# Performance work log

Hardware: AMD Instinct MI355X
Metric: run time of the kernel (lower is better)

## Reference

```python
import jax, jax.numpy as jnp
import numpy as np

S = 7                # feature map size
A = 12               # anchors per cell
N = S * S * A        # 588 total anchors
ANCHOR_SCALES = [0.3, 0.5, 0.7, 0.9]
ANCHOR_RATIOS = [0.7, 1.0, 1.3]
CONF_THR = 0.3
NMS_THR = 0.5
MAX_DET = 100
BN_EPS = 1e-5
DN = ('NCHW', 'OIHW', 'NCHW')


def _anchors():
    g = (jnp.arange(S, dtype=jnp.float32) + 0.5) / S
    cx, cy = jnp.meshgrid(g, g, indexing='ij')
    centers = jnp.stack([cx, cy], -1).reshape(-1, 2)                 # [49,2]
    sc = jnp.asarray(ANCHOR_SCALES, jnp.float32)[:, None]
    rt = jnp.sqrt(jnp.asarray(ANCHOR_RATIOS, jnp.float32))[None, :]
    ws = (sc * rt).reshape(-1)
    hs = (sc / rt).reshape(-1)
    deltas = jnp.stack([-ws, -hs, ws, hs], -1) * 0.5                 # [12,4]
    return (jnp.concatenate([centers, centers], -1)[:, None, :] + deltas[None]).reshape(-1, 4)


def _conv(x, w, b, pad):
    y = jax.lax.conv_general_dilated(x, w, (1, 1), [(pad, pad), (pad, pad)], dimension_numbers=DN)
    return y + b[None, :, None, None]


def _bn_relu(x, g, be, mu, var):
    inv = g * jax.lax.rsqrt(var + BN_EPS)
    return jax.nn.relu(x * inv[None, :, None, None] + (be - mu * inv)[None, :, None, None])


def _decode(box_pred, anchors):
    ac = (anchors[:, :2] + anchors[:, 2:]) * 0.5
    asz = anchors[:, 2:] - anchors[:, :2]
    pc = box_pred[..., :2] * asz + ac
    ps = jnp.exp(box_pred[..., 2:]) * asz
    return jnp.concatenate([pc - ps * 0.5, pc + ps * 0.5], -1)


def _iou(b):
    area = (b[:, 2] - b[:, 0]) * (b[:, 3] - b[:, 1])
    lt = jnp.maximum(b[:, None, :2], b[None, :, :2])
    rb = jnp.minimum(b[:, None, 2:], b[None, :, 2:])
    wh = jnp.clip(rb - lt, 0.0)
    inter = wh[..., 0] * wh[..., 1]
    return inter / (area[:, None] + area[None, :] - inter + 1e-9)


def _nms_single(boxes, scores):
    # greedy NMS, fixed-shape: sort by score, sequentially suppress, pad to MAX_DET
    order = jnp.argsort(-scores)
    bs = boxes[order]
    ss = scores[order]
    vs = ss > CONF_THR
    iou = _iou(bs)
    idx = jnp.arange(N)

    def body(suppr, i):
        keep = vs[i] & jnp.logical_not(suppr[i])
        suppr = suppr | (keep & (iou[i] > NMS_THR) & (idx > i))
        return suppr, keep

    _, keep = jax.lax.scan(body, jnp.zeros((N,), bool), idx)
    kept = jnp.where(keep, ss, -1.0)           # scores in (0,1), -1 is a safe sentinel
    top_s, top_i = jax.lax.top_k(kept, MAX_DET)
    valid = top_s > 0.0
    out_b = jnp.where(valid[:, None], bs[top_i], 0.0)
    out_s = jnp.where(valid, top_s, 0.0)
    return jnp.concatenate([out_b, out_s[:, None], valid.astype(jnp.float32)[:, None]], -1)


def _forward(features, w1, b1, g1, be1, mu1, var1, w2, b2, g2, be2, mu2, var2,
             w3, b3, g3, be3, mu3, var3, w4, b4, g4, be4, mu4, var4,
             w_cls, b_cls, w_box, b_box):
    x = _bn_relu(_conv(features, w1, b1, 0), g1, be1, mu1, var1)   # fpn 1x1
    x = _bn_relu(_conv(x, w2, b2, 1), g2, be2, mu2, var2)          # fpn 3x3
    x = _bn_relu(_conv(x, w3, b3, 1), g3, be3, mu3, var3)          # det_conv 1
    x = _bn_relu(_conv(x, w4, b4, 1), g4, be4, mu4, var4)          # det_conv 2
    B = features.shape[0]
    box = _conv(x, w_box, b_box, 1).transpose(0, 2, 3, 1).reshape(B, -1, 4)
    conf = jax.nn.sigmoid(_conv(x, w_cls, b_cls, 1)).transpose(0, 2, 3, 1).reshape(B, -1)
    boxes = _decode(box, _anchors())
    return jax.vmap(_nms_single)(boxes, conf)   # [B, MAX_DET, 6] = box(4)+score+valid


def setup_inputs() -> dict:
    key = jax.random.key(0)
    ks = iter(jax.random.split(key, 64))
    B = 256
    d = {'features': jax.random.normal(next(ks), (B, 512, S, S), jnp.float32)}
    for n, o, i, k in [('1', 256, 512, 1), ('2', 256, 256, 3), ('3', 256, 256, 3), ('4', 256, 256, 3)]:
        d['w' + n] = 0.01 * jax.random.normal(next(ks), (o, i, k, k), jnp.float32)
        d['b' + n] = jnp.zeros((o,), jnp.float32)
        d['g' + n] = 1.0 + 0.1 * jax.random.normal(next(ks), (o,), jnp.float32)
        d['be' + n] = 0.05 * jax.random.normal(next(ks), (o,), jnp.float32)
        d['mu' + n] = 0.1 * jax.random.normal(next(ks), (o,), jnp.float32)
        d['var' + n] = jax.random.uniform(next(ks), (o,), jnp.float32, 0.5, 1.5)
    d['w_cls'] = 0.01 * jax.random.normal(next(ks), (A, 256, 3, 3), jnp.float32)
    d['b_cls'] = jnp.zeros((A,), jnp.float32)
    d['w_box'] = 0.01 * jax.random.normal(next(ks), (4 * A, 256, 3, 3), jnp.float32)
    d['b_box'] = jnp.zeros((4 * A,), jnp.float32)
    return d


def reference(features, w1, b1, g1, be1, mu1, var1, w2, b2, g2, be2, mu2, var2,
              w3, b3, g3, be3, mu3, var3, w4, b4, g4, be4, mu4, var4,
              w_cls, b_cls, w_box, b_box):
    return _forward(features, w1, b1, g1, be1, mu1, var1, w2, b2, g2, be2, mu2, var2,
                    w3, b3, g3, be3, mu3, var3, w4, b4, g4, be4, mu4, var4,
                    w_cls, b_cls, w_box, b_box)
```

## Files before the change

### kernel.cpp

```cpp
#include <hip/hip_runtime.h>
#include <cmath>
#include <cstdint>

#define NPOS 49
#define NANCH 588

__global__ void transpose_all(
    const float* __restrict__ w1, const float* __restrict__ w2,
    const float* __restrict__ w3, const float* __restrict__ w4,
    const float* __restrict__ wb, const float* __restrict__ wc,
    float* __restrict__ w1t, float* __restrict__ w2t, float* __restrict__ w3t,
    float* __restrict__ w4t, float* __restrict__ wbt, float* __restrict__ wct) {
  int idx = blockIdx.x * blockDim.x + threadIdx.x;
  if (idx < 131072) {
    int o = idx / 512, c = idx % 512;
    w1t[((c >> 2) * 256 + o) * 4 + (c & 3)] = w1[idx];
    return;
  }
  idx -= 131072;
  if (idx < 589824) {
    int o = idx / 2304, ck = idx % 2304, c = ck / 9, k = ck - c * 9;
    w2t[(c * 256 + o) * 12 + k] = w2[idx]; return;
  }
  idx -= 589824;
  if (idx < 589824) {
    int o = idx / 2304, ck = idx % 2304, c = ck / 9, k = ck - c * 9;
    w3t[(c * 256 + o) * 12 + k] = w3[idx]; return;
  }
  idx -= 589824;
  if (idx < 589824) {
    int o = idx / 2304, ck = idx % 2304, c = ck / 9, k = ck - c * 9;
    w4t[(c * 256 + o) * 12 + k] = w4[idx]; return;
  }
  idx -= 589824;
  if (idx < 110592) { int o = idx / 2304, ck = idx % 2304; wbt[ck * 48 + o] = wb[idx]; return; }
  idx -= 110592;
  if (idx < 27648)  { int o = idx / 2304, ck = idx % 2304; wct[ck * 12 + o] = wc[idx]; return; }
}

__global__ __launch_bounds__(512, 1) void conv1x1_bn(
    const float* __restrict__ in, const float* __restrict__ wt_f,
    const float* __restrict__ bias, const float* __restrict__ gg,
    const float* __restrict__ be, const float* __restrict__ mu,
    const float* __restrict__ var, float* __restrict__ out) {
  __shared__ float smem[512 * 52];
  const int b = blockIdx.x, t = threadIdx.x;
  const int slot = t & 127, cg = t >> 7;
  const int o0 = slot, o1 = slot + 128;
  const float* inb = in + (size_t)b * (512 * NPOS);
  const float4* wq = (const float4*)wt_f;
  const int q0 = cg * 32;
  float4 wca = wq[q0 * 256 + o0];
  float4 wcb = wq[q0 * 256 + o1];
  for (int i = t; i < 512 * NPOS; i += 512) {
    int c = i / NPOS, p = i - c * NPOS;
    smem[c * 52 + p] = inb[i];
  }
  float acc0[NPOS], acc1[NPOS];
#pragma unroll
  for (int p = 0; p < NPOS; ++p) { acc0[p] = 0.f; acc1[p] = 0.f; }
  __syncthreads();
  for (int q = q0; q < q0 + 32; ++q) {
    int nq = (q + 1 < q0 + 32) ? q + 1 : q;
    float4 wna = wq[nq * 256 + o0];
    float4 wnb = wq[nq * 256 + o1];
#pragma unroll
    for (int j = 0; j < 4; ++j) {
      float wa = (j == 0) ? wca.x : (j == 1) ? wca.y : (j == 2) ? wca.z : wca.w;
      float wb2 = (j == 0) ? wcb.x : (j == 1) ? wcb.y : (j == 2) ? wcb.z : wcb.w;
      const float* row = smem + (q * 4 + j) * 52;
      const float4* tr = (const float4*)row;
#pragma unroll
      for (int jj = 0; jj < 12; ++jj) {
        float4 qv = tr[jj];
        acc0[4 * jj + 0] = fmaf(wa, qv.x, acc0[4 * jj + 0]);
        acc0[4 * jj + 1] = fmaf(wa, qv.y, acc0[4 * jj + 1]);
        acc0[4 * jj + 2] = fmaf(wa, qv.z, acc0[4 * jj + 2]);
        acc0[4 * jj + 3] = fmaf(wa, qv.w, acc0[4 * jj + 3]);
        acc1[4 * jj + 0] = fmaf(wb2, qv.x, acc1[4 * jj + 0]);
        acc1[4 * jj + 1] = fmaf(wb2, qv.y, acc1[4 * jj + 1]);
        acc1[4 * jj + 2] = fmaf(wb2, qv.z, acc1[4 * jj + 2]);
        acc1[4 * jj + 3] = fmaf(wb2, qv.w, acc1[4 * jj + 3]);
      }
      float s48 = row[48];
      acc0[48] = fmaf(wa, s48, acc0[48]);
      acc1[48] = fmaf(wb2, s48, acc1[48]);
    }
    wca = wna; wcb = wnb;
  }
  __syncthreads();
  float* P0 = smem;
  float* P1 = smem + 12544;
  if (cg == 1) {
#pragma unroll
    for (int p = 0; p < NPOS; ++p) { P0[(slot * 2 + 0) * NPOS + p] = acc0[p]; P0[(slot * 2 + 1) * NPOS + p] = acc1[p]; }
  }
  if (cg == 3) {
#pragma unroll
    for (int p = 0; p < NPOS; ++p) { P1[(slot * 2 + 0) * NPOS + p] = acc0[p]; P1[(slot * 2 + 1) * NPOS + p] = acc1[p]; }
  }
  __syncthreads();
  if (cg == 0) {
#pragma unroll
    for (int p = 0; p < NPOS; ++p) { acc0[p] += P0[(slot * 2 + 0) * NPOS + p]; acc1[p] += P0[(slot * 2 + 1) * NPOS + p]; }
  }
  if (cg == 2) {
#pragma unroll
    for (int p = 0; p < NPOS; ++p) { acc0[p] += P1[(slot * 2 + 0) * NPOS + p]; acc1[p] += P1[(slot * 2 + 1) * NPOS + p]; }
  }
  __syncthreads();
  if (cg == 2) {
#pragma unroll
    for (int p = 0; p < NPOS; ++p) { P0[(slot * 2 + 0) * NPOS + p] = acc0[p]; P0[(slot * 2 + 1) * NPOS + p] = acc1[p]; }
  }
  __syncthreads();
  if (cg == 0) {
    float sc0 = gg[o0] / sqrtf(var[o0] + 1e-5f);
    float ad0 = (bias[o0] - mu[o0]) * sc0 + be[o0];
    float sc1 = gg[o1] / sqrtf(var[o1] + 1e-5f);
    float ad1 = (bias[o1] - mu[o1]) * sc1 + be[o1];
#pragma unroll
    for (int p = 0; p < NPOS; ++p) {
      float v0 = (acc0[p] + P0[(slot * 2 + 0) * NPOS + p]) * sc0 + ad0;
      float v1 = (acc1[p] + P0[(slot * 2 + 1) * NPOS + p]) * sc1 + ad1;
      P1[o0 * NPOS + p] = v0 > 0.f ? v0 : 0.f;
      P1[o1 * NPOS + p] = v1 > 0.f ? v1 : 0.f;
    }
  }
  __syncthreads();
  float* outb = out + (size_t)b * (256 * NPOS);
  for (int i = t; i < 256 * NPOS; i += 512) outb[i] = P1[i];
}

#define LOADROW(dst, base, rr)                                          \
  do {                                                                  \
    const float4* q4_ = (const float4*)((base) + (rr) * 12);            \
    float4 q0_ = q4_[0], q1_ = q4_[1], q2_ = q4_[2];                    \
    dst[0] = q0_.x; dst[1] = q0_.y; dst[2] = q0_.z; dst[3] = q0_.w;     \
    dst[4] = q1_.x; dst[5] = q1_.y; dst[6] = q1_.z; dst[7] = q1_.w;     \
    dst[8] = q2_.x;                                                     \
  } while (0)

__global__ __launch_bounds__(512, 1) void conv3x3_bn(
    const float* __restrict__ in, const float* __restrict__ wt,
    const float* __restrict__ bias, const float* __restrict__ gg,
    const float* __restrict__ be, const float* __restrict__ mu,
    const float* __restrict__ var, float* __restrict__ out) {
  __shared__ float smem[256 * 108];
  const int b = blockIdx.x, t = threadIdx.x;
  const int slot = t & 127, cg = t >> 7;
  const int o0 = slot, o1 = slot + 128;
  const float* inb = in + (size_t)b * (256 * NPOS);
  float4* z4 = (float4*)smem;
  for (int i = t; i < 6912; i += 512) z4[i] = make_float4(0.f, 0.f, 0.f, 0.f);
  const int c0 = cg * 64;
  const float4* wv4 = (const float4*)wt;
  float4 wa0 = wv4[(c0 * 256 + o0) * 3 + 0];
  float4 wa1 = wv4[(c0 * 256 + o0) * 3 + 1];
  float4 wa2 = wv4[(c0 * 256 + o0) * 3 + 2];
  float4 wb0 = wv4[(c0 * 256 + o1) * 3 + 0];
  float4 wb1 = wv4[(c0 * 256 + o1) * 3 + 1];
  float4 wb2 = wv4[(c0 * 256 + o1) * 3 + 2];
  __syncthreads();
  for (int i = t; i < 256 * NPOS; i += 512) {
    int c = i / NPOS, p = i - c * NPOS, y = p / 7, x = p - y * 7;
    smem[c * 108 + (y + 1) * 12 + (x + 1)] = inb[i];
  }
  float acc0[NPOS], acc1[NPOS];
#pragma unroll
  for (int p = 0; p < NPOS; ++p) { acc0[p] = 0.f; acc1[p] = 0.f; }
  __syncthreads();
  for (int cl = 0; cl < 64; ++cl) {
    const int c = c0 + cl;
    const int cn = (cl + 1 < 64) ? c + 1 : c;
    float4 na0 = wv4[(cn * 256 + o0) * 3 + 0];
    float4 na1 = wv4[(cn * 256 + o0) * 3 + 1];
    float4 na2 = wv4[(cn * 256 + o0) * 3 + 2];
    float4 nb0 = wv4[(cn * 256 + o1) * 3 + 0];
    float4 nb1 = wv4[(cn * 256 + o1) * 3 + 1];
    float4 nb2 = wv4[(cn * 256 + o1) * 3 + 2];
    const float* tb = smem + c * 108;
    float R[3][9];
    LOADROW(R[0], tb, 0);
    LOADROW(R[1], tb, 1);
#pragma unroll
    for (int y = 0; y < 7; ++y) {
      LOADROW(R[(y + 2) % 3], tb, y + 2);
      const float* r0 = R[y % 3];
      const float* r1 = R[(y + 1) % 3];
      const float* r2 = R[(y + 2) % 3];
#pragma unroll
      for (int x = 0; x < 7; ++x) {
        float s0 = acc0[y * 7 + x];
        s0 = fmaf(wa0.x, r0[x],     s0);
        s0 = fmaf(wa0.y, r0[x + 1], s0);
        s0 = fmaf(wa0.z, r0[x + 2], s0);
        s0 = fmaf(wa0.w, r1[x],     s0);
        s0 = fmaf(wa1.x, r1[x + 1], s0);
        s0 = fmaf(wa1.y, r1[x + 2], s0);
        s0 = fmaf(wa1.z, r2[x],     s0);
        s0 = fmaf(wa1.w, r2[x + 1], s0);
        s0 = fmaf(wa2.x, r2[x + 2], s0);
        acc0[y * 7 + x] = s0;
        float s1 = acc1[y * 7 + x];
        s1 = fmaf(wb0.x, r0[x],     s1);
        s1 = fmaf(wb0.y, r0[x + 1], s1);
        s1 = fmaf(wb0.z, r0[x + 2], s1);
        s1 = fmaf(wb0.w, r1[x],     s1);
        s1 = fmaf(wb1.x, r1[x + 1], s1);
        s1 = fmaf(wb1.y, r1[x + 2], s1);
        s1 = fmaf(wb1.z, r2[x],     s1);
        s1 = fmaf(wb1.w, r2[x + 1], s1);
        s1 = fmaf(wb2.x, r2[x + 2], s1);
        acc1[y * 7 + x] = s1;
      }
    }
    wa0 = na0; wa1 = na1; wa2 = na2;
    wb0 = nb0; wb1 = nb1; wb2 = nb2;
  }
  __syncthreads();
  float* P0 = smem;
  float* P1 = smem + 12544;
  if (cg == 1) {
#pragma unroll
    for (int p = 0; p < NPOS; ++p) { P0[(slot * 2 + 0) * NPOS + p] = acc0[p]; P0[(slot * 2 + 1) * NPOS + p] = acc1[p]; }
  }
  if (cg == 3) {
#pragma unroll
    for (int p = 0; p < NPOS; ++p) { P1[(slot * 2 + 0) * NPOS + p] = acc0[p]; P1[(slot * 2 + 1) * NPOS + p] = acc1[p]; }
  }
  __syncthreads();
  if (cg == 0) {
#pragma unroll
    for (int p = 0; p < NPOS; ++p) { acc0[p] += P0[(slot * 2 + 0) * NPOS + p]; acc1[p] += P0[(slot * 2 + 1) * NPOS + p]; }
  }
  if (cg == 2) {
#pragma unroll
    for (int p = 0; p < NPOS; ++p) { acc0[p] += P1[(slot * 2 + 0) * NPOS + p]; acc1[p] += P1[(slot * 2 + 1) * NPOS + p]; }
  }
  __syncthreads();
  if (cg == 2) {
#pragma unroll
    for (int p = 0; p < NPOS; ++p) { P0[(slot * 2 + 0) * NPOS + p] = acc0[p]; P0[(slot * 2 + 1) * NPOS + p] = acc1[p]; }
  }
  __syncthreads();
  if (cg == 0) {
    float sc0 = gg[o0] / sqrtf(var[o0] + 1e-5f);
    float ad0 = (bias[o0] - mu[o0]) * sc0 + be[o0];
    float sc1 = gg[o1] / sqrtf(var[o1] + 1e-5f);
    float ad1 = (bias[o1] - mu[o1]) * sc1 + be[o1];
#pragma unroll
    for (int p = 0; p < NPOS; ++p) {
      float v0 = (acc0[p] + P0[(slot * 2 + 0) * NPOS + p]) * sc0 + ad0;
      float v1 = (acc1[p] + P0[(slot * 2 + 1) * NPOS + p]) * sc1 + ad1;
      P1[o0 * NPOS + p] = v0 > 0.f ? v0 : 0.f;
      P1[o1 * NPOS + p] = v1 > 0.f ? v1 : 0.f;
    }
  }
  __syncthreads();
  float* outb = out + (size_t)b * (256 * NPOS);
  for (int i = t; i < 256 * NPOS; i += 512) outb[i] = P1[i];
}

__global__ __launch_bounds__(512, 2) void heads_decode(
    const float* __restrict__ in, const float* __restrict__ wbt,
    const float* __restrict__ wct, const float* __restrict__ bb,
    const float* __restrict__ bc, float* __restrict__ BXg,
    float* __restrict__ SCg) {
  __shared__ float smem[256 * 108];
  const int b = blockIdx.x, t = threadIdx.x;
  for (int i = t; i < 256 * 108; i += 512) smem[i] = 0.f;
  __syncthreads();
  const float* inb = in + (size_t)b * (256 * NPOS);
  for (int i = t; i < 256 * NPOS; i += 512) {
    int c = i / NPOS, p = i - c * NPOS, y = p / 7, x = p - y * 7;
    smem[c * 108 + (y + 1) * 12 + (x + 1)] = inb[i];
  }
  __syncthreads();
  float acc[NPOS];
#pragma unroll
  for (int p = 0; p < NPOS; ++p) acc[p] = 0.f;
  int o = 0, cg = 0;
  if (t < 480) {
    o = t % 60; cg = t / 60;
    const float* wbase; int wstr;
    if (o < 48) { wbase = wbt + o; wstr = 48; }
    else        { wbase = wct + (o - 48); wstr = 12; }
    const int c0 = cg * 32;
    float wc_[9];
#pragma unroll
    for (int k = 0; k < 9; ++k) wc_[k] = wbase[(c0 * 9 + k) * wstr];
    for (int c = c0; c < c0 + 32; ++c) {
      int cn = (c + 1 < c0 + 32) ? c + 1 : c;
      float wn_[9];
#pragma unroll
      for (int k = 0; k < 9; ++k) wn_[k] = wbase[(cn * 9 + k) * wstr];
      const float* tb = smem + c * 108;
      float R[3][9];
      LOADROW(R[0], tb, 0);
      LOADROW(R[1], tb, 1);
#pragma unroll
      for (int y = 0; y < 7; ++y) {
        LOADROW(R[(y + 2) % 3], tb, y + 2);
        const float* r0 = R[y % 3];
        const float* r1 = R[(y + 1) % 3];
        const float* r2 = R[(y + 2) % 3];
#pragma unroll
        for (int x = 0; x < 7; ++x) {
          float s = acc[y * 7 + x];
          s = fmaf(wc_[0], r0[x], s);
          s = fmaf(wc_[1], r0[x + 1], s);
          s = fmaf(wc_[2], r0[x + 2], s);
          s = fmaf(wc_[3], r1[x], s);
          s = fmaf(wc_[4], r1[x + 1], s);
          s = fmaf(wc_[5], r1[x + 2], s);
          s = fmaf(wc_[6], r2[x], s);
          s = fmaf(wc_[7], r2[x + 1], s);
          s = fmaf(wc_[8], r2[x + 2], s);
          acc[y * 7 + x] = s;
        }
      }
#pragma unroll
      for (int k = 0; k < 9; ++k) wc_[k] = wn_[k];
    }
  }
  __syncthreads();
  float* part = smem;
  float* H = smem + 7 * 2940;
  if (t < 480 && cg > 0) {
#pragma unroll
    for (int p = 0; p < NPOS; ++p) part[(cg - 1) * 2940 + o * NPOS + p] = acc[p];
  }
  __syncthreads();
  if (t < 60) {
    float bsum = (o < 48) ? bb[o] : bc[o - 48];
#pragma unroll
    for (int p = 0; p < NPOS; ++p) {
      float v = acc[p] + bsum;
      for (int g = 0; g < 7; ++g) v += part[g * 2940 + o * NPOS + p];
      H[o * NPOS + p] = v;
    }
  }
  __syncthreads();
  const float scl[4] = {0.3f, 0.5f, 0.7f, 0.9f};
  const float rat[3] = {0.7f, 1.0f, 1.3f};
  for (int n = t; n < NANCH; n += 512) {
    int p = n / 12, a = n - p * 12;
    int ph = p / 7, pw = p - ph * 7;
    float cx = (ph + 0.5f) / 7.0f;
    float cy = (pw + 0.5f) / 7.0f;
    int s = a / 3, r = a - s * 3;
    float rt = sqrtf(rat[r]);
    float wsz = scl[s] * rt, hsz = scl[s] / rt;
    float x1 = cx + (-wsz) * 0.5f, y1 = cy + (-hsz) * 0.5f;
    float x2 = cx + wsz * 0.5f,    y2 = cy + hsz * 0.5f;
    float acx = (x1 + x2) * 0.5f,  acy = (y1 + y2) * 0.5f;
    float asx = x2 - x1,           asy = y2 - y1;
    float bp0 = H[(a * 4 + 0) * NPOS + p];
    float bp1 = H[(a * 4 + 1) * NPOS + p];
    float bp2 = H[(a * 4 + 2) * NPOS + p];
    float bp3 = H[(a * 4 + 3) * NPOS + p];
    float pcx = bp0 * asx + acx;
    float pcy = bp1 * asy + acy;
    float psx = expf(bp2) * asx;
    float psy = expf(bp3) * asy;
    float* bx = BXg + (size_t)b * (NANCH * 4) + n * 4;
    bx[0] = pcx - psx * 0.5f;
    bx[1] = pcy - psy * 0.5f;
    bx[2] = pcx + psx * 0.5f;
    bx[3] = pcy + psy * 0.5f;
    float lg = H[(48 + a) * NPOS + p];
    SCg[(size_t)b * NANCH + n] = 1.0f / (1.0f + expf(-lg));
  }
}

__device__ inline unsigned long long shfl64(unsigned long long v, int lane) {
  int lo = __shfl((int)(unsigned)(v & 0xffffffffULL), lane, 64);
  int hi = __shfl((int)(unsigned)(v >> 32), lane, 64);
  return ((unsigned long long)(unsigned)hi << 32) | (unsigned)lo;
}

__global__ __launch_bounds__(512, 4) void nms_kernel(
    const float* __restrict__ BXg, const float* __restrict__ SCg,
    float* __restrict__ out) {
  __shared__ float smem[16576];
  unsigned long long* KEY = (unsigned long long*)smem;
  float* SB  = smem + 1176;
  float* SSc = smem + 3528;
  float* AR  = smem + 4116;
  unsigned long long* ADJ = (unsigned long long*)(smem + 4704);
  int* KEEP = (int*)(smem + 16464);
  int* CNT  = (int*)(smem + 16564);
  const int b = blockIdx.x, t = threadIdx.x;
  const float* scb = SCg + (size_t)b * NANCH;
  const float4* bxb = (const float4*)(BXg + (size_t)b * (NANCH * 4));
  for (int i = t; i < NANCH; i += 512) {
    unsigned u = __float_as_uint(scb[i]);
    u = (u & 0x80000000u) ? ~u : (u | 0x80000000u);
    u = ~u;
    KEY[i] = ((unsigned long long)u << 32) | (unsigned)i;
  }
  __syncthreads();
  for (int i = t; i < NANCH; i += 512) {
    unsigned long long k = KEY[i];
    int rank = 0;
    for (int j = 0; j < NANCH; ++j) rank += (KEY[j] < k) ? 1 : 0;
    float4 bx = bxb[i];
    ((float4*)SB)[rank] = bx;
    SSc[rank] = scb[i];
    AR[rank] = (bx.z - bx.x) * (bx.w - bx.y);
  }
  __syncthreads();
  const float4* SB4 = (const float4*)SB;
  for (int task = t; task < NANCH * 10; task += 512) {
    int i = task % NANCH, w = task / NANCH;
    float4 a = SB4[i];
    float aar = AR[i];
    int jbase = w * 64;
    int jend = NANCH - jbase; if (jend > 64) jend = 64;
    unsigned long long bits = 0;
    for (int bi = 0; bi < jend; ++bi) {
      int j = jbase + bi;
      float4 bb = SB4[j];
      float ltx = fmaxf(a.x, bb.x), lty = fmaxf(a.y, bb.y);
      float rbx = fminf(a.z, bb.z), rby = fminf(a.w, bb.w);
      float wx = rbx - ltx; wx = wx > 0.f ? wx : 0.f;
      float wy = rby - lty; wy = wy > 0.f ? wy : 0.f;
      float inter = wx * wy;
      float iou = inter / (aar + AR[j] - inter + 1e-9f);
      if (iou > 0.5f) bits |= (1ULL << bi);
    }
    ADJ[i * 10 + w] = bits;
  }
  __syncthreads();
  if (t < 64) {
    unsigned long long valid = 0, supp = 0;
    if (t < 10) {
      int jbase = t * 64;
      int jend = NANCH - jbase; if (jend > 64) jend = 64;
      for (int k = 0; k < jend; ++k)
        valid |= (unsigned long long)(SSc[jbase + k] > 0.3f ? 1 : 0) << k;
    }
    int cnt = 0;
    for (int w = 0; w < 10 && cnt < 100; ++w) {
      unsigned long long cur = shfl64(valid, w) & ~shfl64(supp, w);
      while (cur && cnt < 100) {
        int bpos = (int)__builtin_ctzll(cur);
        int i = w * 64 + bpos;
        if (t == 0) KEEP[cnt] = i;
        cnt++;
        unsigned long long a = (t < 10) ? ADJ[i * 10 + t] : 0ULL;
        if (t < w) a = 0ULL;
        else if (t == w) a &= ~((2ULL << bpos) - 1ULL);
        supp |= a;
        unsigned long long aw = shfl64(a, w);
        cur &= ~aw;
        cur &= ~(1ULL << bpos);
      }
    }
    if (t == 0) *CNT = cnt;
  }
  __syncthreads();
  int cnt = *CNT;
  if (t < 100) {
    float4 bx = make_float4(0.f, 0.f, 0.f, 0.f);
    float s = 0.f, vld = 0.f;
    if (t < cnt) {
      int i = KEEP[t];
      bx = SB4[i];
      s = SSc[i];
      vld = 1.f;
    }
    float* ob = out + (size_t)b * 600 + t * 6;
    ob[0] = bx.x; ob[1] = bx.y; ob[2] = bx.z; ob[3] = bx.w;
    ob[4] = s;    ob[5] = vld;
  }
}

extern "C" void kernel_launch(void* const* d_in, const int* in_sizes, int n_in,
                              void* d_out, int out_size, void* d_ws, size_t ws_size,
                              hipStream_t stream) {
  const float* feat = (const float*)d_in[0];
  const float* w1  = (const float*)d_in[1];
  const float* b1  = (const float*)d_in[2];
  const float* g1  = (const float*)d_in[3];
  const float* be1 = (const float*)d_in[4];
  const float* mu1 = (const float*)d_in[5];
  const float* v1  = (const float*)d_in[6];
  const float* w2  = (const float*)d_in[7];
  const float* b2  = (const float*)d_in[8];
  const float* g2  = (const float*)d_in[9];
  const float* be2 = (const float*)d_in[10];
  const float* mu2 = (const float*)d_in[11];
  const float* v2  = (const float*)d_in[12];
  const float* w3  = (const float*)d_in[13];
  const float* b3  = (const float*)d_in[14];
  const float* g3  = (const float*)d_in[15];
  const float* be3 = (const float*)d_in[16];
  const float* mu3 = (const float*)d_in[17];
  const float* v3  = (const float*)d_in[18];
  const float* w4  = (const float*)d_in[19];
  const float* b4  = (const float*)d_in[20];
  const float* g4  = (const float*)d_in[21];
  const float* be4 = (const float*)d_in[22];
  const float* mu4 = (const float*)d_in[23];
  const float* v4  = (const float*)d_in[24];
  const float* wcls = (const float*)d_in[25];
  const float* bcls = (const float*)d_in[26];
  const float* wbox = (const float*)d_in[27];
  const float* bbox = (const float*)d_in[28];

  const int B = in_sizes[0] / (512 * NPOS);
  float* ws  = (float*)d_ws;
  size_t xsz = (size_t)B * 256 * NPOS;
  float* xa  = ws;
  float* xb  = xa + xsz;
  float* w1t = xb + xsz;
  float* w2t = w1t + 131072;
  float* w3t = w2t + 786432;
  float* w4t = w3t + 786432;
  float* wbt = w4t + 786432;
  float* wct = wbt + 110592;
  float* BXg = wct + 27648;
  float* SCg = BXg + (size_t)B * (NANCH * 4);

  transpose_all<<<(2038784 + 255) / 256, 256, 0, stream>>>(
      w1, w2, w3, w4, wbox, wcls, w1t, w2t, w3t, w4t, wbt, wct);
  conv1x1_bn<<<B, 512, 0, stream>>>(feat, w1t, b1, g1, be1, mu1, v1, xa);
  conv3x3_bn<<<B, 512, 0, stream>>>(xa, w2t, b2, g2, be2, mu2, v2, xb);
  conv3x3_bn<<<B, 512, 0, stream>>>(xb, w3t, b3, g3, be3, mu3, v3, xa);
  conv3x3_bn<<<B, 512, 0, stream>>>(xa, w4t, b4, g4, be4, mu4, v4, xb);
  heads_decode<<<B, 512, 0, stream>>>(xb, wbt, wct, bbox, bcls, BXg, SCg);
  nms_kernel<<<B, 512, 0, stream>>>(BXg, SCg, (float*)d_out);
}
```

Before: 895.9 us.

## Split 3x3 conv output channels across two blocks with compact unpadded smem tiles

The 3x3 conv kernel now launches two blocks per image, each computing 128 output channels, so every thread holds one 49-element accumulator instead of two. Input tiles are stored unpadded at an 8-float row stride, with the left halo inserted in registers and the top and bottom rows handled by peeled loops. This roughly halves shared memory and register use per block, allowing two blocks per CU under launch_bounds(512,2) and doubling grid parallelism. The cost is that each image's input is staged into shared memory twice, and each thread now does half as many FMAs per shared-memory row load.

```diff
diff --git a/kernel.cpp b/kernel.cpp
--- a/kernel.cpp
+++ b/kernel.cpp
@@ -132,6 +132,129 @@
   for (int i = t; i < 256 * NPOS; i += 512) outb[i] = P1[i];
 }
 
+#define LOADROW2(dst, base, yy)                                         \
+  do {                                                                  \
+    const float4* q4_ = (const float4*)((base) + (yy) * 8);             \
+    float4 a_ = q4_[0], b_ = q4_[1];                                    \
+    dst[0] = 0.f;                                                       \
+    dst[1] = a_.x; dst[2] = a_.y; dst[3] = a_.z; dst[4] = a_.w;         \
+    dst[5] = b_.x; dst[6] = b_.y; dst[7] = b_.z; dst[8] = b_.w;         \
+  } while (0)
+
+#define FMA9(accbase, rt, rc, rb)                                       \
+  do {                                                                  \
+    _Pragma("unroll")                                                   \
+    for (int x = 0; x < 7; ++x) {                                       \
+      float s = acc[(accbase) + x];                                     \
+      s = fmaf(wa0.x, rt[x],     s);                                    \
+      s = fmaf(wa0.y, rt[x + 1], s);                                    \
+      s = fmaf(wa0.z, rt[x + 2], s);                                    \
+      s = fmaf(wa0.w, rc[x],     s);                                    \
+      s = fmaf(wa1.x, rc[x + 1], s);                                    \
+      s = fmaf(wa1.y, rc[x + 2], s);                                    \
+      s = fmaf(wa1.z, rb[x],     s);                                    \
+      s = fmaf(wa1.w, rb[x + 1], s);                                    \
+      s = fmaf(wa2.x, rb[x + 2], s);                                    \
+      acc[(accbase) + x] = s;                                           \
+    }                                                                   \
+  } while (0)
+
+__global__ __launch_bounds__(512, 2) void conv3x3_bn(
+    const float* __restrict__ in, const float* __restrict__ wt,
+    const float* __restrict__ bias, const float* __restrict__ gg,
+    const float* __restrict__ be, const float* __restrict__ mu,
+    const float* __restrict__ var, float* __restrict__ out) {
+  __shared__ float smem[256 * 56];
+  const int blk = blockIdx.x, t = threadIdx.x;
+  const int b = blk >> 1, oh = blk & 1;
+  const int slot = t & 127, cg = t >> 7;
+  const int og = oh * 128 + slot;
+  const float* inb = in + (size_t)b * (256 * NPOS);
+  float4* z4 = (float4*)smem;
+  for (int i = t; i < 3584; i += 512) z4[i] = make_float4(0.f, 0.f, 0.f, 0.f);
+  const int c0 = cg * 64;
+  const float4* wv4 = (const float4*)wt;
+  float4 wa0 = wv4[(c0 * 256 + og) * 3 + 0];
+  float4 wa1 = wv4[(c0 * 256 + og) * 3 + 1];
+  float4 wa2 = wv4[(c0 * 256 + og) * 3 + 2];
+  __syncthreads();
+  for (int i = t; i < 256 * NPOS; i += 512) {
+    int c = i / NPOS, p = i - c * NPOS, y = p / 7, x = p - y * 7;
+    smem[c * 56 + y * 8 + x] = inb[i];
+  }
+  float acc[NPOS];
+#pragma unroll
+  for (int p = 0; p < NPOS; ++p) acc[p] = 0.f;
+  __syncthreads();
+  for (int cl = 0; cl < 64; ++cl) {
+    const int c = c0 + cl;
+    const int cn = (cl + 1 < 64) ? c + 1 : c;
+    float4 na0 = wv4[(cn * 256 + og) * 3 + 0];
+    float4 na1 = wv4[(cn * 256 + og) * 3 + 1];
+    float4 na2 = wv4[(cn * 256 + og) * 3 + 2];
+    const float* tb = smem + c * 56;
+    float R0[9], R1[9], R2[9];
+    LOADROW2(R0, tb, 0);
+    LOADROW2(R1, tb, 1);
+#pragma unroll
+    for (int x = 0; x < 7; ++x) {
+      float s = acc[x];
+      s = fmaf(wa0.w, R0[x],     s);
+      s = fmaf(wa1.x, R0[x + 1], s);
+      s = fmaf(wa1.y, R0[x + 2], s);
+      s = fmaf(wa1.z, R1[x],     s);
+      s = fmaf(wa1.w, R1[x + 1], s);
+      s = fmaf(wa2.x, R1[x + 2], s);
+      acc[x] = s;
+    }
+    LOADROW2(R2, tb, 2);
+    FMA9(7, R0, R1, R2);
+    LOADROW2(R0, tb, 3);
+    FMA9(14, R1, R2, R0);
+    LOADROW2(R1, tb, 4);
+    FMA9(21, R2, R0, R1);
+    LOADROW2(R2, tb, 5);
+    FMA9(28, R0, R1, R2);
+    LOADROW2(R0, tb, 6);
+    FMA9(35, R1, R2, R0);
+#pragma unroll
+    for (int x = 0; x < 7; ++x) {
+      float s = acc[42 + x];
+      s = fmaf(wa0.x, R2[x],     s);
+      s = fmaf(wa0.y, R2[x + 1], s);
+      s = fmaf(wa0.z, R2[x + 2], s);
+      s = fmaf(wa0.w, R0[x],     s);
+      s = fmaf(wa1.x, R0[x + 1], s);
+      s = fmaf(wa1.y, R0[x + 2], s);
+      acc[42 + x] = s;
+    }
+    wa0 = na0; wa1 = na1; wa2 = na2;
+  }
+  __syncthreads();
+  float* P0 = smem;
+  float* P1 = smem + 6272;
+  if (cg == 1) { for (int p = 0; p < NPOS; ++p) P0[slot * NPOS + p] = acc[p]; }
+  if (cg == 3) { for (int p = 0; p < NPOS; ++p) P1[slot * NPOS + p] = acc[p]; }
+  __syncthreads();
+  if (cg == 0) { for (int p = 0; p < NPOS; ++p) acc[p] += P0[slot * NPOS + p]; }
+  if (cg == 2) { for (int p = 0; p < NPOS; ++p) acc[p] += P1[slot * NPOS + p]; }
+  __syncthreads();
+  if (cg == 2) { for (int p = 0; p < NPOS; ++p) P0[slot * NPOS + p] = acc[p]; }
+  __syncthreads();
+  if (cg == 0) {
+    float scale = gg[og] / sqrtf(var[og] + 1e-5f);
+    float add = (bias[og] - mu[og]) * scale + be[og];
+#pragma unroll
+    for (int p = 0; p < NPOS; ++p) {
+      float v = (acc[p] + P0[slot * NPOS + p]) * scale + add;
+      P1[slot * NPOS + p] = v > 0.f ? v : 0.f;
+    }
+  }
+  __syncthreads();
+  float* outb = out + (size_t)b * (256 * NPOS) + oh * (128 * NPOS);
+  for (int i = t; i < 128 * NPOS; i += 512) outb[i] = P1[i];
+}
+
 #define LOADROW(dst, base, rr)                                          \
   do {                                                                  \
     const float4* q4_ = (const float4*)((base) + (rr) * 12);            \
@@ -140,127 +263,6 @@
     dst[4] = q1_.x; dst[5] = q1_.y; dst[6] = q1_.z; dst[7] = q1_.w;     \
     dst[8] = q2_.x;                                                     \
   } while (0)
-
-__global__ __launch_bounds__(512, 1) void conv3x3_bn(
-    const float* __restrict__ in, const float* __restrict__ wt,
-    const float* __restrict__ bias, const float* __restrict__ gg,
-    const float* __restrict__ be, const float* __restrict__ mu,
-    const float* __restrict__ var, float* __restrict__ out) {
-  __shared__ float smem[256 * 108];
-  const int b = blockIdx.x, t = threadIdx.x;
-  const int slot = t & 127, cg = t >> 7;
-  const int o0 = slot, o1 = slot + 128;
-  const float* inb = in + (size_t)b * (256 * NPOS);
-  float4* z4 = (float4*)smem;
-  for (int i = t; i < 6912; i += 512) z4[i] = make_float4(0.f, 0.f, 0.f, 0.f);
-  const int c0 = cg * 64;
-  const float4* wv4 = (const float4*)wt;
-  float4 wa0 = wv4[(c0 * 256 + o0) * 3 + 0];
-  float4 wa1 = wv4[(c0 * 256 + o0) * 3 + 1];
-  float4 wa2 = wv4[(c0 * 256 + o0) * 3 + 2];
-  float4 wb0 = wv4[(c0 * 256 + o1) * 3 + 0];
-  float4 wb1 = wv4[(c0 * 256 + o1) * 3 + 1];
-  float4 wb2 = wv4[(c0 * 256 + o1) * 3 + 2];
-  __syncthreads();
-  for (int i = t; i < 256 * NPOS; i += 512) {
-    int c = i / NPOS, p = i - c * NPOS, y = p / 7, x = p - y * 7;
-    smem[c * 108 + (y + 1) * 12 + (x + 1)] = inb[i];
-  }
-  float acc0[NPOS], acc1[NPOS];
-#pragma unroll
-  for (int p = 0; p < NPOS; ++p) { acc0[p] = 0.f; acc1[p] = 0.f; }
-  __syncthreads();
-  for (int cl = 0; cl < 64; ++cl) {
-    const int c = c0 + cl;
-    const int cn = (cl + 1 < 64) ? c + 1 : c;
-    float4 na0 = wv4[(cn * 256 + o0) * 3 + 0];
-    float4 na1 = wv4[(cn * 256 + o0) * 3 + 1];
-    float4 na2 = wv4[(cn * 256 + o0) * 3 + 2];
-    float4 nb0 = wv4[(cn * 256 + o1) * 3 + 0];
-    float4 nb1 = wv4[(cn * 256 + o1) * 3 + 1];
-    float4 nb2 = wv4[(cn * 256 + o1) * 3 + 2];
-    const float* tb = smem + c * 108;
-    float R[3][9];
-    LOADROW(R[0], tb, 0);
-    LOADROW(R[1], tb, 1);
-#pragma unroll
-    for (int y = 0; y < 7; ++y) {
-      LOADROW(R[(y + 2) % 3], tb, y + 2);
-      const float* r0 = R[y % 3];
-      const float* r1 = R[(y + 1) % 3];
-      const float* r2 = R[(y + 2) % 3];
-#pragma unroll
-      for (int x = 0; x < 7; ++x) {
-        float s0 = acc0[y * 7 + x];
-        s0 = fmaf(wa0.x, r0[x],     s0);
-        s0 = fmaf(wa0.y, r0[x + 1], s0);
-        s0 = fmaf(wa0.z, r0[x + 2], s0);
-        s0 = fmaf(wa0.w, r1[x],     s0);
-        s0 = fmaf(wa1.x, r1[x + 1], s0);
-        s0 = fmaf(wa1.y, r1[x + 2], s0);
-        s0 = fmaf(wa1.z, r2[x],     s0);
-        s0 = fmaf(wa1.w, r2[x + 1], s0);
-        s0 = fmaf(wa2.x, r2[x + 2], s0);
-        acc0[y * 7 + x] = s0;
-        float s1 = acc1[y * 7 + x];
-        s1 = fmaf(wb0.x, r0[x],     s1);
-        s1 = fmaf(wb0.y, r0[x + 1], s1);
-        s1 = fmaf(wb0.z, r0[x + 2], s1);
-        s1 = fmaf(wb0.w, r1[x],     s1);
-        s1 = fmaf(wb1.x, r1[x + 1], s1);
-        s1 = fmaf(wb1.y, r1[x + 2], s1);
-        s1 = fmaf(wb1.z, r2[x],     s1);
-        s1 = fmaf(wb1.w, r2[x + 1], s1);
-        s1 = fmaf(wb2.x, r2[x + 2], s1);
-        acc1[y * 7 + x] = s1;
-      }
-    }
-    wa0 = na0; wa1 = na1; wa2 = na2;
-    wb0 = nb0; wb1 = nb1; wb2 = nb2;
-  }
-  __syncthreads();
-  float* P0 = smem;
-  float* P1 = smem + 12544;
-  if (cg == 1) {
-#pragma unroll
-    for (int p = 0; p < NPOS; ++p) { P0[(slot * 2 + 0) * NPOS + p] = acc0[p]; P0[(slot * 2 + 1) * NPOS + p] = acc1[p]; }
-  }
-  if (cg == 3) {
-#pragma unroll
-    for (int p = 0; p < NPOS; ++p) { P1[(slot * 2 + 0) * NPOS + p] = acc0[p]; P1[(slot * 2 + 1) * NPOS + p] = acc1[p]; }
-  }
-  __syncthreads();
-  if (cg == 0) {
-#pragma unroll
-    for (int p = 0; p < NPOS; ++p) { acc0[p] += P0[(slot * 2 + 0) * NPOS + p]; acc1[p] += P0[(slot * 2 + 1) * NPOS + p]; }
-  }
-  if (cg == 2) {
-#pragma unroll
-    for (int p = 0; p < NPOS; ++p) { acc0[p] += P1[(slot * 2 + 0) * NPOS + p]; acc1[p] += P1[(slot * 2 + 1) * NPOS + p]; }
-  }
-  __syncthreads();
-  if (cg == 2) {
-#pragma unroll
-    for (int p = 0; p < NPOS; ++p) { P0[(slot * 2 + 0) * NPOS + p] = acc0[p]; P0[(slot * 2 + 1) * NPOS + p] = acc1[p]; }
-  }
-  __syncthreads();
-  if (cg == 0) {
-    float sc0 = gg[o0] / sqrtf(var[o0] + 1e-5f);
-    float ad0 = (bias[o0] - mu[o0]) * sc0 + be[o0];
-    float sc1 = gg[o1] / sqrtf(var[o1] + 1e-5f);
-    float ad1 = (bias[o1] - mu[o1]) * sc1 + be[o1];
-#pragma unroll
-    for (int p = 0; p < NPOS; ++p) {
-      float v0 = (acc0[p] + P0[(slot * 2 + 0) * NPOS + p]) * sc0 + ad0;
-      float v1 = (acc1[p] + P0[(slot * 2 + 1) * NPOS + p]) * sc1 + ad1;
-      P1[o0 * NPOS + p] = v0 > 0.f ? v0 : 0.f;
-      P1[o1 * NPOS + p] = v1 > 0.f ? v1 : 0.f;
-    }
-  }
-  __syncthreads();
-  float* outb = out + (size_t)b * (256 * NPOS);
-  for (int i = t; i < 256 * NPOS; i += 512) outb[i] = P1[i];
-}
 
 __global__ __launch_bounds__(512, 2) void heads_decode(
     const float* __restrict__ in, const float* __restrict__ wbt,
@@ -527,9 +529,9 @@
   transpose_all<<<(2038784 + 255) / 256, 256, 0, stream>>>(
       w1, w2, w3, w4, wbox, wcls, w1t, w2t, w3t, w4t, wbt, wct);
   conv1x1_bn<<<B, 512, 0, stream>>>(feat, w1t, b1, g1, be1, mu1, v1, xa);
-  conv3x3_bn<<<B, 512, 0, stream>>>(xa, w2t, b2, g2, be2, mu2, v2, xb);
-  conv3x3_bn<<<B, 512, 0, stream>>>(xb, w3t, b3, g3, be3, mu3, v3, xa);
-  conv3x3_bn<<<B, 512, 0, stream>>>(xa, w4t, b4, g4, be4, mu4, v4, xb);
+  conv3x3_bn<<<2 * B, 512, 0, stream>>>(xa, w2t, b2, g2, be2, mu2, v2, xb);
+  conv3x3_bn<<<2 * B, 512, 0, stream>>>(xb, w3t, b3, g3, be3, mu3, v3, xa);
+  conv3x3_bn<<<2 * B, 512, 0, stream>>>(xa, w4t, b4, g4, be4, mu4, v4, xb);
   heads_decode<<<B, 512, 0, stream>>>(xb, wbt, wct, bbox, bcls, BXg, SCg);
   nms_kernel<<<B, 512, 0, stream>>>(BXg, SCg, (float*)d_out);
 }
```

Result: faster. 848.6 us (-5.3%).
